# Performance work log

Hardware: AMD Instinct MI355X
Metric: run time of the kernel (lower is better)

The kernel has to match this reference:

```python
import jax, jax.numpy as jnp
import numpy as np

WS = 10      # window_size
HID = 32     # hidden_dim
B, T = 1024, 4096


def setup_inputs() -> dict:
    key = jax.random.key(0)
    k = jax.random.split(key, 7)
    returns = jax.random.normal(k[0], (B, T), dtype=jnp.float32) * 0.01
    W1 = jax.random.normal(k[1], (WS, HID), dtype=jnp.float32) * (1.0 / np.sqrt(WS))
    b1 = jnp.zeros((HID,), dtype=jnp.float32)
    W2 = jax.random.normal(k[2], (HID, HID), dtype=jnp.float32) * (1.0 / np.sqrt(HID))
    b2 = jnp.zeros((HID,), dtype=jnp.float32)
    W3 = jax.random.normal(k[3], (HID, 1), dtype=jnp.float32) * (1.0 / np.sqrt(HID))
    b3 = jnp.zeros((1,), dtype=jnp.float32)
    return {"returns": returns, "W1": W1, "b1": b1, "W2": W2, "b2": b2, "W3": W3, "b3": b3}


def reference(returns, W1, b1, W2, b2, W3, b3):
    ws = W1.shape[0]
    Bb, Tt = returns.shape
    # Unfold all sliding windows at once: windows[b, i, :] = returns[b, i:i+ws]
    # (window ending just before timestep t = i + ws)
    idx = jnp.arange(Tt - ws)[:, None] + jnp.arange(ws)[None, :]  # [T-ws, ws]
    windows = returns[:, idx]                                     # [B, T-ws, ws]
    h = jax.nn.relu(windows @ W1 + b1)                            # [B, T-ws, HID]
    h = jax.nn.relu(h @ W2 + b2)                                  # [B, T-ws, HID]
    out = 0.5 * jax.nn.sigmoid((h @ W3 + b3).squeeze(-1))         # [B, T-ws]
    # H_local[:, t] = out[:, t-ws] for t >= ws; first ws columns copy column ws
    head = jnp.broadcast_to(out[:, :1], (Bb, ws))                 # [B, ws]
    return jnp.concatenate([head, out], axis=1)                   # [B, T]
```

## Files before the change

### kernel.cpp

```cpp
#include <hip/hip_runtime.h>
#include <math.h>

typedef _Float16 f16x8  __attribute__((ext_vector_type(8)));
typedef _Float16 h2v    __attribute__((ext_vector_type(2)));
typedef float    f32x16 __attribute__((ext_vector_type(16)));
typedef float    f32x4  __attribute__((ext_vector_type(4)));
typedef __fp16   h2a    __attribute__((ext_vector_type(2)));
typedef unsigned u32x4  __attribute__((ext_vector_type(4)));

#define WS    10
#define HID   32
#define BDIM  256
#define NWAVE 4
#define GN    32
#define T_LEN 4096
#define NGRP  (T_LEN / GN)

__device__ inline unsigned pack2u(float a, float b) {
    h2a t = __builtin_amdgcn_cvt_pkrtz(a, b);
    return __builtin_bit_cast(unsigned, t);
}
__device__ inline unsigned relu2(unsigned u) {
    h2v x = __builtin_bit_cast(h2v, u);
    h2v z = {(_Float16)0.0f, (_Float16)0.0f};
    return __builtin_bit_cast(unsigned, __builtin_elementwise_max(x, z));
}

__global__ __launch_bounds__(BDIM, 4)
void hurst_row(const float* __restrict__ returns,
               const float* __restrict__ W1, const float* __restrict__ b1,
               const float* __restrict__ W2, const float* __restrict__ b2,
               const float* __restrict__ W3, const float* __restrict__ b3,
               float* __restrict__ out)
{
    const int tid  = threadIdx.x;
    const int wid  = tid >> 6;
    const int lane = tid & 63;
    const int n    = lane & 31;
    const int hi   = lane >> 5;
    const int permidx = (lane ^ 32) << 2;

    f32x16 b1v, b2v, w3v;
    #pragma unroll
    for (int i = 0; i < 4; ++i) {
        const f32x4 v1 = ((const f32x4*)b1)[2 * i + hi];
        const f32x4 v2 = ((const f32x4*)b2)[2 * i + hi];
        const f32x4 v3 = ((const f32x4*)W3)[2 * i + hi];
        #pragma unroll
        for (int o = 0; o < 4; ++o) {
            b1v[4 * i + o] = v1[o];
            b2v[4 * i + o] = v2[o];
            w3v[4 * i + o] = v3[o];
        }
    }
    const float b3s = b3[0];

    f16x8 a1, a2lo, a2hi;
    #pragma unroll
    for (int jj = 0; jj < 8; ++jj) {
        const int k  = 8 * hi + jj;
        a1[jj] = (k < WS) ? (_Float16)W1[k * HID + n] : (_Float16)0.0f;
        const int kf = (k & 3) | ((k & 4) << 1) | ((k & 8) >> 1);
        a2lo[jj] = (_Float16)W2[kf * HID + n];
        a2hi[jj] = (_Float16)W2[(16 + kf) * HID + n];
    }

    const float* rptr = returns + (size_t)blockIdx.x * T_LEN;
    float*       optr = out     + (size_t)blockIdx.x * T_LEN;

    for (int g = wid; g < NGRP; g += NWAVE) {
        const int t  = g * GN + n;
        const int ws = (t >= WS) ? (t - WS) : 0;

        u32x4 xu;
        if (hi == 0) {
            float w8[8];
            __builtin_memcpy(w8, &rptr[ws], 32);
            xu[0] = pack2u(w8[0], w8[1]);
            xu[1] = pack2u(w8[2], w8[3]);
            xu[2] = pack2u(w8[4], w8[5]);
            xu[3] = pack2u(w8[6], w8[7]);
        } else {
            float w2[2];
            __builtin_memcpy(w2, &rptr[ws + 8], 8);
            xu[0] = pack2u(w2[0], w2[1]);
            xu[1] = 0u; xu[2] = 0u; xu[3] = 0u;
        }
        const f16x8 xb = __builtin_bit_cast(f16x8, xu);

        f32x16 d1 = __builtin_amdgcn_mfma_f32_32x32x16_f16(a1, xb, b1v, 0, 0, 0);

        u32x4 blo_u, bhi_u;
        #pragma unroll
        for (int i = 0; i < 4; ++i) {
            blo_u[i] = relu2(pack2u(d1[2 * i],     d1[2 * i + 1]));
            bhi_u[i] = relu2(pack2u(d1[8 + 2 * i], d1[9 + 2 * i]));
        }

        f32x16 d2 = __builtin_amdgcn_mfma_f32_32x32x16_f16(
                        a2lo, __builtin_bit_cast(f16x8, blo_u), b2v, 0, 0, 0);
        d2 = __builtin_amdgcn_mfma_f32_32x32x16_f16(
                        a2hi, __builtin_bit_cast(f16x8, bhi_u), d2, 0, 0, 0);

        float acc = 0.0f;
        #pragma unroll
        for (int r = 0; r < 16; ++r)
            acc = fmaf(fmaxf(d2[r], 0.0f), w3v[r], acc);
        acc += __builtin_bit_cast(float,
                 __builtin_amdgcn_ds_bpermute(permidx, __builtin_bit_cast(int, acc)));

        const float o = 0.5f * __builtin_amdgcn_rcpf(1.0f + __expf(-(acc + b3s)));
        if (hi == 0)
            optr[t] = o;
    }
}

extern "C" void kernel_launch(void* const* d_in, const int* in_sizes, int n_in,
                              void* d_out, int out_size, void* d_ws, size_t ws_size,
                              hipStream_t stream) {
    const float* returns = (const float*)d_in[0];
    const float* W1      = (const float*)d_in[1];
    const float* b1      = (const float*)d_in[2];
    const float* W2      = (const float*)d_in[3];
    const float* b2      = (const float*)d_in[4];
    const float* W3      = (const float*)d_in[5];
    const float* b3      = (const float*)d_in[6];
    float* out = (float*)d_out;

    const int B = out_size / T_LEN;

    dim3 grid(B, 1, 1);
    dim3 block(BDIM, 1, 1);
    hurst_row<<<grid, block, 0, stream>>>(returns, W1, b1, W2, b2, W3, b3, out);
}
```

Baseline: 106.7 us.

## Move output layer onto MFMA and software-prefetch next window loads

Replaces the per-lane FMA reduction plus ds_bpermute cross-half sum for the final 32->1 layer with two extra MFMA ops, using W3 broadcast across all output rows and b3 as the accumulator init. It also prefetches the next iteration's input window into registers while the current one is computed, and makes the loads branch-free for both lane halves. The intent is to cut VALU work and LDS-permute latency and to hide global load latency. The cost is two more MFMAs per group, extra registers for the prefetched values, and fp16 rounding of the layer-2 activations before the last dot product.

```diff
diff --git a/kernel.cpp b/kernel.cpp
--- a/kernel.cpp
+++ b/kernel.cpp
@@ -27,35 +27,34 @@
 }
 
 __global__ __launch_bounds__(BDIM, 4)
-void hurst_row(const float* __restrict__ returns,
-               const float* __restrict__ W1, const float* __restrict__ b1,
-               const float* __restrict__ W2, const float* __restrict__ b2,
-               const float* __restrict__ W3, const float* __restrict__ b3,
-               float* __restrict__ out)
+void hurst_row5(const float* __restrict__ returns,
+                const float* __restrict__ W1, const float* __restrict__ b1,
+                const float* __restrict__ W2, const float* __restrict__ b2,
+                const float* __restrict__ W3, const float* __restrict__ b3,
+                float* __restrict__ out)
 {
     const int tid  = threadIdx.x;
     const int wid  = tid >> 6;
     const int lane = tid & 63;
     const int n    = lane & 31;
     const int hi   = lane >> 5;
-    const int permidx = (lane ^ 32) << 2;
 
-    f32x16 b1v, b2v, w3v;
+    f32x16 b1v, b2v, b3v;
     #pragma unroll
     for (int i = 0; i < 4; ++i) {
         const f32x4 v1 = ((const f32x4*)b1)[2 * i + hi];
         const f32x4 v2 = ((const f32x4*)b2)[2 * i + hi];
-        const f32x4 v3 = ((const f32x4*)W3)[2 * i + hi];
         #pragma unroll
         for (int o = 0; o < 4; ++o) {
             b1v[4 * i + o] = v1[o];
             b2v[4 * i + o] = v2[o];
-            w3v[4 * i + o] = v3[o];
         }
     }
     const float b3s = b3[0];
+    #pragma unroll
+    for (int r = 0; r < 16; ++r) b3v[r] = b3s;
 
-    f16x8 a1, a2lo, a2hi;
+    f16x8 a1, a2lo, a2hi, a3lo, a3hi;
     #pragma unroll
     for (int jj = 0; jj < 8; ++jj) {
         const int k  = 8 * hi + jj;
@@ -63,55 +62,68 @@
         const int kf = (k & 3) | ((k & 4) << 1) | ((k & 8) >> 1);
         a2lo[jj] = (_Float16)W2[kf * HID + n];
         a2hi[jj] = (_Float16)W2[(16 + kf) * HID + n];
+        a3lo[jj] = (_Float16)W3[kf];
+        a3hi[jj] = (_Float16)W3[16 + kf];
     }
 
     const float* rptr = returns + (size_t)blockIdx.x * T_LEN;
     float*       optr = out     + (size_t)blockIdx.x * T_LEN;
 
+    const int t0  = wid * GN + n;
+    int ws_c = (t0 >= WS) ? (t0 - WS) : 0;
+    float e2_c[2], v6_c[6];
+    __builtin_memcpy(e2_c, &rptr[ws_c + 8 * hi], 8);
+    __builtin_memcpy(v6_c, &rptr[ws_c + 2], 24);
+
     for (int g = wid; g < NGRP; g += NWAVE) {
-        const int t  = g * GN + n;
-        const int ws = (t >= WS) ? (t - WS) : 0;
+        const int gn_ = (g + NWAVE < NGRP) ? (g + NWAVE) : g;
+        const int tn  = gn_ * GN + n;
+        const int wsn = (tn >= WS) ? (tn - WS) : 0;
+        float e2_n[2], v6_n[6];
+        __builtin_memcpy(e2_n, &rptr[wsn + 8 * hi], 8);
+        __builtin_memcpy(v6_n, &rptr[wsn + 2], 24);
 
         u32x4 xu;
-        if (hi == 0) {
-            float w8[8];
-            __builtin_memcpy(w8, &rptr[ws], 32);
-            xu[0] = pack2u(w8[0], w8[1]);
-            xu[1] = pack2u(w8[2], w8[3]);
-            xu[2] = pack2u(w8[4], w8[5]);
-            xu[3] = pack2u(w8[6], w8[7]);
-        } else {
-            float w2[2];
-            __builtin_memcpy(w2, &rptr[ws + 8], 8);
-            xu[0] = pack2u(w2[0], w2[1]);
-            xu[1] = 0u; xu[2] = 0u; xu[3] = 0u;
-        }
+        xu[0] = pack2u(e2_c[0], e2_c[1]);
+        xu[1] = hi ? 0u : pack2u(v6_c[0], v6_c[1]);
+        xu[2] = hi ? 0u : pack2u(v6_c[2], v6_c[3]);
+        xu[3] = hi ? 0u : pack2u(v6_c[4], v6_c[5]);
         const f16x8 xb = __builtin_bit_cast(f16x8, xu);
 
         f32x16 d1 = __builtin_amdgcn_mfma_f32_32x32x16_f16(a1, xb, b1v, 0, 0, 0);
 
-        u32x4 blo_u, bhi_u;
+        u32x4 p1lo, p1hi;
         #pragma unroll
         for (int i = 0; i < 4; ++i) {
-            blo_u[i] = relu2(pack2u(d1[2 * i],     d1[2 * i + 1]));
-            bhi_u[i] = relu2(pack2u(d1[8 + 2 * i], d1[9 + 2 * i]));
+            p1lo[i] = relu2(pack2u(d1[2 * i],     d1[2 * i + 1]));
+            p1hi[i] = relu2(pack2u(d1[8 + 2 * i], d1[9 + 2 * i]));
         }
 
         f32x16 d2 = __builtin_amdgcn_mfma_f32_32x32x16_f16(
-                        a2lo, __builtin_bit_cast(f16x8, blo_u), b2v, 0, 0, 0);
+                        a2lo, __builtin_bit_cast(f16x8, p1lo), b2v, 0, 0, 0);
         d2 = __builtin_amdgcn_mfma_f32_32x32x16_f16(
-                        a2hi, __builtin_bit_cast(f16x8, bhi_u), d2, 0, 0, 0);
+                        a2hi, __builtin_bit_cast(f16x8, p1hi), d2, 0, 0, 0);
 
-        float acc = 0.0f;
+        u32x4 p2lo, p2hi;
         #pragma unroll
-        for (int r = 0; r < 16; ++r)
-            acc = fmaf(fmaxf(d2[r], 0.0f), w3v[r], acc);
-        acc += __builtin_bit_cast(float,
-                 __builtin_amdgcn_ds_bpermute(permidx, __builtin_bit_cast(int, acc)));
+        for (int i = 0; i < 4; ++i) {
+            p2lo[i] = relu2(pack2u(d2[2 * i],     d2[2 * i + 1]));
+            p2hi[i] = relu2(pack2u(d2[8 + 2 * i], d2[9 + 2 * i]));
+        }
 
-        const float o = 0.5f * __builtin_amdgcn_rcpf(1.0f + __expf(-(acc + b3s)));
+        f32x16 d3 = __builtin_amdgcn_mfma_f32_32x32x16_f16(
+                        a3lo, __builtin_bit_cast(f16x8, p2lo), b3v, 0, 0, 0);
+        d3 = __builtin_amdgcn_mfma_f32_32x32x16_f16(
+                        a3hi, __builtin_bit_cast(f16x8, p2hi), d3, 0, 0, 0);
+
+        const float o = 0.5f * __builtin_amdgcn_rcpf(1.0f + __expf(-d3[0]));
         if (hi == 0)
-            optr[t] = o;
+            optr[g * GN + n] = o;
+
+        #pragma unroll
+        for (int i = 0; i < 2; ++i) e2_c[i] = e2_n[i];
+        #pragma unroll
+        for (int i = 0; i < 6; ++i) v6_c[i] = v6_n[i];
     }
 }
 
@@ -131,5 +143,5 @@
 
     dim3 grid(B, 1, 1);
     dim3 block(BDIM, 1, 1);
-    hurst_row<<<grid, block, 0, stream>>>(returns, W1, b1, W2, b2, W3, b3, out);
+    hurst_row5<<<grid, block, 0, stream>>>(returns, W1, b1, W2, b2, W3, b3, out);
 }
```

Measured after the change: 101.8 us. 4.6% less time.
